# Optimization experiments

Measured on AMD Instinct MI355X. Metric: run time of the kernel, lower is better.

Reference implementation:

```python
import jax, jax.numpy as jnp
import numpy as np

K = 512
HIDDEN = 256


def setup_inputs() -> dict:
    key = jax.random.key(0)
    k1, k2 = jax.random.split(key)
    z = jax.random.normal(k1, (8, 8192, HIDDEN), dtype=jnp.float32)
    # codebook init: uniform(-1/k, 1/k) as in the torch module
    codebook = jax.random.uniform(k2, (K, HIDDEN), dtype=jnp.float32,
                                  minval=-1.0 / K, maxval=1.0 / K)
    return {"z": z, "codebook": codebook}


def reference(z, codebook):
    # squared L2 distance to every code, expanded form to avoid the
    # [N, k, hidden] intermediate: ||z||^2 - 2 z.c + ||c||^2
    z2 = jnp.sum(z * z, axis=-1, keepdims=True)            # [B, T, 1]
    c2 = jnp.sum(codebook * codebook, axis=-1)             # [k]
    cross = jnp.einsum('bth,kh->btk', z, codebook)         # [B, T, k]
    distances = z2 - 2.0 * cross + c2                      # [B, T, k]
    ind = jnp.argmin(distances, axis=-1)                   # [B, T] int
    z_q = codebook[ind]                                    # [B, T, hidden]

    vq_loss = jnp.mean((z_q - jax.lax.stop_gradient(z)) ** 2)
    commitment_loss = jnp.mean((z - jax.lax.stop_gradient(z_q)) ** 2)
    z_q_st = z + jax.lax.stop_gradient(z_q - z)
    return (z_q_st, ind, vq_loss + commitment_loss)
```

## Files before the change

### kernel.cpp

```cpp
#include <hip/hip_runtime.h>

#define M_TOKENS 65536
#define HID      256
#define KCODES   512

#define IND_OFF  (M_TOKENS * HID)
#define LOSS_OFF (IND_OFF + M_TOKENS)

#define TAU      1.5e-4f

#define WS_C2_OFF        16
#define WS_BHI_OFF       4096
#define WS_BLO_OFF       (4096 + 262144)
#define WS_LIST_OFF_FAST (4096 + 524288)
#define WS_LIST_OFF_SLOW 4096
#define WS_MIN_FAST      (WS_LIST_OFF_FAST + 8192 * 4)

typedef __attribute__((ext_vector_type(8))) short  short8;
typedef __attribute__((ext_vector_type(4))) float  f32x4;

__device__ inline unsigned short f2bf(float f) {
    unsigned u = __float_as_uint(f);
    u += 0x7FFF + ((u >> 16) & 1);
    return (unsigned short)(u >> 16);
}
__device__ inline float bf2f(unsigned short h) {
    return __uint_as_float(((unsigned)h) << 16);
}

__global__ __launch_bounds__(256) void vq_prep(
    const float* __restrict__ cb,
    unsigned short* __restrict__ Bhi, unsigned short* __restrict__ Blo,
    float* __restrict__ c2, double* __restrict__ acc, int* __restrict__ cnt) {
    int b = blockIdx.x;
    if (b < 64) {
        int g = b * 256 + threadIdx.x;
        int frag = g >> 6, lane = g & 63;
        int nb = frag >> 3, kb = frag & 7;
        int code = nb * 16 + (lane & 15);
        int kk = kb * 32 + (lane >> 4) * 8;
        const float4* s4 = reinterpret_cast<const float4*>(cb + code * HID + kk);
        float4 v0 = s4[0], v1 = s4[1];
        float f[8] = {v0.x, v0.y, v0.z, v0.w, v1.x, v1.y, v1.z, v1.w};
        short8 vh, vl;
        #pragma unroll
        for (int j = 0; j < 8; ++j) {
            unsigned short h = f2bf(f[j]);
            vh[j] = (short)h;
            vl[j] = (short)f2bf(f[j] - bf2f(h));
        }
        *reinterpret_cast<short8*>(Bhi + (size_t)g * 8) = vh;
        *reinterpret_cast<short8*>(Blo + (size_t)g * 8) = vl;
    } else {
        if (b == 64 && threadIdx.x == 0) { *acc = 0.0; *cnt = 0; }
        int k = (b - 64) * 256 + threadIdx.x;
        const float* row = cb + k * HID;
        double s = 0.0;
        for (int i = 0; i < HID; ++i) {
            double v = (double)row[i];
            s = fma(v, v, s);
        }
        c2[k] = (float)s;
    }
}

__global__ __launch_bounds__(256, 2) void vq_main_mfma(
    const float* __restrict__ z, const float* __restrict__ cb,
    const float* __restrict__ c2g,
    const unsigned short* __restrict__ Bhi,
    const unsigned short* __restrict__ Blo,
    float* __restrict__ out, double* __restrict__ loss_acc,
    int* __restrict__ cnt, int* __restrict__ list, int cap) {

    __shared__ short8 ldsB[2][32][64];
    __shared__ float  lds_c2[KCODES];

    const int tid  = threadIdx.x;
    const int wid  = tid >> 6;
    const int lane = tid & 63;
    const int q    = lane >> 4;
    const int tokW = blockIdx.x * 128 + wid * 32;

    const float4* z4  = reinterpret_cast<const float4*>(z);
    const float4* cb4 = reinterpret_cast<const float4*>(cb);

    lds_c2[tid]       = c2g[tid];
    lds_c2[tid + 256] = c2g[tid + 256];

#define STAGE(kv, bufv) do {                                                   \
        _Pragma("unroll")                                                      \
        for (int j = 0; j < 8; ++j) {                                          \
            int s_  = (wid << 3) | j;                                          \
            int g_  = s_ >> 4;                                                 \
            int t_  = s_ & 15;                                                 \
            int kb_ = t_ & 7;                                                  \
            const unsigned short* src_ =                                       \
                ((t_ < 8) ? Bhi : Blo) +                                       \
                (((size_t)((2 * (kv) + g_) * 8 + kb_) * 64 + lane) << 3);      \
            __builtin_amdgcn_global_load_lds(                                  \
                (const __attribute__((address_space(1))) void*)src_,           \
                (__attribute__((address_space(3))) void*)&ldsB[bufv][s_][0],   \
                16, 0, 0);                                                     \
        }                                                                      \
    } while (0)

    STAGE(0, 0);

    short8 ah[2][8], al[2][8];
    float sq[2];
    #pragma unroll
    for (int mf = 0; mf < 2; ++mf) {
        int token = tokW + mf * 16 + (lane & 15);
        const float4* zr = z4 + (size_t)token * 64 + q * 2;
        float s = 0.f;
        #pragma unroll
        for (int kb = 0; kb < 8; ++kb) {
            float4 v0 = zr[kb * 8];
            float4 v1 = zr[kb * 8 + 1];
            float f[8] = {v0.x, v0.y, v0.z, v0.w, v1.x, v1.y, v1.z, v1.w};
            short8 vh, vl;
            #pragma unroll
            for (int j = 0; j < 8; ++j) {
                unsigned short h = f2bf(f[j]);
                vh[j] = (short)h;
                vl[j] = (short)f2bf(f[j] - bf2f(h));
                s = fmaf(f[j], f[j], s);
            }
            ah[mf][kb] = vh;
            al[mf][kb] = vl;
        }
        s += __shfl_xor(s, 16, 64);
        s += __shfl_xor(s, 32, 64);
        sq[mf] = s;
    }

    float b1[2][4], b2[2][4];
    int   i1[2][4];
    #pragma unroll
    for (int mf = 0; mf < 2; ++mf)
        #pragma unroll
        for (int r = 0; r < 4; ++r) { b1[mf][r] = 3.4e38f; b2[mf][r] = 3.4e38f; i1[mf][r] = 0; }

    #pragma unroll 2
    for (int k = 0; k < 16; ++k) {
        int buf = k & 1;
        __syncthreads();
        if (k < 15) STAGE(k + 1, buf ^ 1);

        #pragma unroll
        for (int g = 0; g < 2; ++g) {
            f32x4 a0 = {0.f, 0.f, 0.f, 0.f};
            f32x4 a1 = {0.f, 0.f, 0.f, 0.f};
            __builtin_amdgcn_s_setprio(1);
            #pragma unroll
            for (int kb = 0; kb < 8; ++kb) {
                short8 vbh = ldsB[buf][g * 16 + kb][lane];
                short8 vbl = ldsB[buf][g * 16 + 8 + kb][lane];
                a0 = __builtin_amdgcn_mfma_f32_16x16x32_bf16(ah[0][kb], vbh, a0, 0, 0, 0);
                a1 = __builtin_amdgcn_mfma_f32_16x16x32_bf16(ah[1][kb], vbh, a1, 0, 0, 0);
                a0 = __builtin_amdgcn_mfma_f32_16x16x32_bf16(al[0][kb], vbh, a0, 0, 0, 0);
                a1 = __builtin_amdgcn_mfma_f32_16x16x32_bf16(al[1][kb], vbh, a1, 0, 0, 0);
                a0 = __builtin_amdgcn_mfma_f32_16x16x32_bf16(ah[0][kb], vbl, a0, 0, 0, 0);
                a1 = __builtin_amdgcn_mfma_f32_16x16x32_bf16(ah[1][kb], vbl, a1, 0, 0, 0);
            }
            __builtin_amdgcn_s_setprio(0);
            int code = (2 * k + g) * 16 + (lane & 15);
            float c2v = lds_c2[code];
            #pragma unroll
            for (int r = 0; r < 4; ++r) {
                float s0 = fmaf(-2.f, a0[r], c2v);
                if (s0 < b1[0][r]) { b2[0][r] = b1[0][r]; b1[0][r] = s0; i1[0][r] = code; }
                else if (s0 < b2[0][r]) b2[0][r] = s0;
                float s1 = fmaf(-2.f, a1[r], c2v);
                if (s1 < b1[1][r]) { b2[1][r] = b1[1][r]; b1[1][r] = s1; i1[1][r] = code; }
                else if (s1 < b2[1][r]) b2[1][r] = s1;
            }
        }
    }
#undef STAGE

    #pragma unroll
    for (int st = 1; st <= 8; st <<= 1) {
        #pragma unroll
        for (int mf = 0; mf < 2; ++mf)
            #pragma unroll
            for (int r = 0; r < 4; ++r) {
                float ob1 = __shfl_xor(b1[mf][r], st, 64);
                int   oi1 = __shfl_xor(i1[mf][r], st, 64);
                float ob2 = __shfl_xor(b2[mf][r], st, 64);
                if (ob1 < b1[mf][r] || (ob1 == b1[mf][r] && oi1 < i1[mf][r])) {
                    b2[mf][r] = fminf(b1[mf][r], ob2);
                    b1[mf][r] = ob1;
                    i1[mf][r] = oi1;
                } else {
                    b2[mf][r] = fminf(b2[mf][r], ob1);
                }
            }
    }

    if ((lane & 15) == 0) {
        #pragma unroll
        for (int mf = 0; mf < 2; ++mf) {
            float4 iv;
            #pragma unroll
            for (int r = 0; r < 4; ++r) {
                ((float*)&iv)[r] = (float)i1[mf][r];
                if (b2[mf][r] - b1[mf][r] <= TAU) {
                    int pos = atomicAdd(cnt, 1);
                    if (pos < cap) list[pos] = tokW + mf * 16 + q * 4 + r;
                }
            }
            *reinterpret_cast<float4*>(out + IND_OFF + tokW + mf * 16 + q * 4) = iv;
        }
    }

    double lsum = 0.0;
    #pragma unroll
    for (int mf = 0; mf < 2; ++mf)
        #pragma unroll
        for (int r = 0; r < 4; ++r) {
            float z2r = __shfl(sq[mf], (lane & 48) | (q * 4 + r), 64);
            if ((lane & 15) == 0) lsum += (double)z2r + (double)b1[mf][r];
        }
    lsum += __shfl_xor(lsum, 16, 64);
    lsum += __shfl_xor(lsum, 32, 64);
    if (lane == 0) atomicAdd(loss_acc, lsum);

    float4* out4 = reinterpret_cast<float4*>(out);
    #pragma unroll
    for (int tt = 0; tt < 32; ++tt) {
        int code = __shfl(i1[tt >> 4][tt & 3], ((tt >> 2) & 3) * 16, 64);
        float4 cv = cb4[(size_t)code * 64 + lane];
        out4[(size_t)(tokW + tt) * 64 + lane] = cv;
    }
}

#define BM   128
#define NC   128
#define KS   32
#define PAD  33

__global__ void vq_init(const float* __restrict__ cb, float* __restrict__ c2,
                        double* __restrict__ acc, int* __restrict__ cnt) {
    int k = threadIdx.x;
    if (k == 0) { *acc = 0.0; *cnt = 0; }
    const float* row = cb + k * HID;
    double s = 0.0;
    for (int i = 0; i < HID; ++i) {
        double v = (double)row[i];
        s = fma(v, v, s);
    }
    c2[k] = (float)s;
}

__global__ __launch_bounds__(256, 2) void vq_main_f32(
    const float* __restrict__ z, const float* __restrict__ cb,
    const float* __restrict__ c2g, float* __restrict__ out,
    double* __restrict__ loss_acc, int* __restrict__ cnt,
    int* __restrict__ list, int cap) {

    __shared__ float smem[(BM + NC) * PAD];
    float* zs = smem;
    float* cs = smem + BM * PAD;

    const int tid = threadIdx.x;
    const int tx = tid & 15;
    const int ty = tid >> 4;
    const int tokBase = blockIdx.x * BM;

    const float4* z4g  = reinterpret_cast<const float4*>(z);
    const float4* cb4g = reinterpret_cast<const float4*>(cb);

    float bs[8], bs2[8];
    int   bi[8];
    #pragma unroll
    for (int m = 0; m < 8; ++m) { bs[m] = 3.4e38f; bs2[m] = 3.4e38f; bi[m] = 0; }

    for (int chunk = 0; chunk < KCODES / NC; ++chunk) {
        float acc[8][8];
        #pragma unroll
        for (int m = 0; m < 8; ++m)
            #pragma unroll
            for (int n = 0; n < 8; ++n) acc[m][n] = 0.f;

        for (int ks = 0; ks < HID / KS; ++ks) {
            __syncthreads();
            #pragma unroll
            for (int i = 0; i < 4; ++i) {
                int f   = tid + i * 256;
                int row = f >> 3;
                int k4  = f & 7;
                float4 zv = z4g[(tokBase + row) * (HID / 4) + ks * (KS / 4) + k4];
                int b = row * PAD + k4 * 4;
                zs[b + 0] = zv.x; zs[b + 1] = zv.y; zs[b + 2] = zv.z; zs[b + 3] = zv.w;
                float4 cv = cb4g[(chunk * NC + row) * (HID / 4) + ks * (KS / 4) + k4];
                cs[b + 0] = cv.x; cs[b + 1] = cv.y; cs[b + 2] = cv.z; cs[b + 3] = cv.w;
            }
            __syncthreads();

            #pragma unroll 2
            for (int k = 0; k < KS; ++k) {
                float zf[8], cf[8];
                #pragma unroll
                for (int m = 0; m < 8; ++m) zf[m] = zs[(ty * 8 + m) * PAD + k];
                #pragma unroll
                for (int n = 0; n < 8; ++n) cf[n] = cs[(tx * 8 + n) * PAD + k];
                #pragma unroll
                for (int m = 0; m < 8; ++m)
                    #pragma unroll
                    for (int n = 0; n < 8; ++n)
                        acc[m][n] = fmaf(zf[m], cf[n], acc[m][n]);
            }
        }

        #pragma unroll
        for (int n = 0; n < 8; ++n) {
            int code = chunk * NC + tx * 8 + n;
            float c2v = c2g[code];
            #pragma unroll
            for (int m = 0; m < 8; ++m) {
                float s = fmaf(-2.f, acc[m][n], c2v);
                if (s < bs[m]) { bs2[m] = bs[m]; bs[m] = s; bi[m] = code; }
                else if (s < bs2[m]) bs2[m] = s;
            }
        }
    }

    __syncthreads();
    float* rs   = smem;
    int*   ri   = reinterpret_cast<int*>(smem + BM * 16);
    float* rs2  = smem + BM * 32;
    int*   inds = reinterpret_cast<int*>(smem + BM * 48);
    float* wred = smem + BM * 48 + BM;

    #pragma unroll
    for (int m = 0; m < 8; ++m) {
        int tok = ty * 8 + m;
        rs [tok * 16 + tx] = bs[m];
        ri [tok * 16 + tx] = bi[m];
        rs2[tok * 16 + tx] = bs2[m];
    }
    __syncthreads();

    if (tid < BM) {
        float B1 = rs[tid * 16];
        int   I1 = ri[tid * 16];
        float B2 = rs2[tid * 16];
        for (int j = 1; j < 16; ++j) {
            float b1v = rs [tid * 16 + j];
            int   i1v = ri [tid * 16 + j];
            float b2v = rs2[tid * 16 + j];
            if (b1v < B1 || (b1v == B1 && i1v < I1)) {
                B2 = fminf(B1, b2v); B1 = b1v; I1 = i1v;
            } else {
                B2 = fminf(B2, b1v);
            }
        }
        inds[tid] = I1;
        out[IND_OFF + tokBase + tid] = (float)I1;
        if (B2 - B1 <= TAU) {
            int pos = atomicAdd(cnt, 1);
            if (pos < cap) list[pos] = tokBase + tid;
        }
    }
    __syncthreads();

    float loc = 0.f;
    float4* out4 = reinterpret_cast<float4*>(out);
    for (int it = 0; it < (BM * HID / 4) / 256; ++it) {
        int e4  = it * 256 + tid;
        int tok = e4 >> 6;
        int h4  = e4 & 63;
        int code = inds[tok];
        float4 cv = cb4g[code * 64 + h4];
        float4 zv = z4g[(tokBase + tok) * 64 + h4];
        out4[(tokBase + tok) * 64 + h4] = cv;
        float dx = cv.x - zv.x, dy = cv.y - zv.y;
        float dz = cv.z - zv.z, dw = cv.w - zv.w;
        loc = fmaf(dx, dx, loc);
        loc = fmaf(dy, dy, loc);
        loc = fmaf(dz, dz, loc);
        loc = fmaf(dw, dw, loc);
    }
    #pragma unroll
    for (int off = 32; off > 0; off >>= 1) loc += __shfl_xor(loc, off, 64);
    int wave = tid >> 6;
    if ((tid & 63) == 0) wred[wave] = loc;
    __syncthreads();
    if (tid == 0) {
        double t = (double)wred[0] + (double)wred[1] +
                   (double)wred[2] + (double)wred[3];
        atomicAdd(loss_acc, t);
    }
}

__global__ __launch_bounds__(256) void vq_refine(
    const float* __restrict__ z, const float* __restrict__ cb,
    const float* __restrict__ c2g, const double* __restrict__ loss_acc,
    const int* __restrict__ cnt, const int* __restrict__ list,
    float* __restrict__ out, int cap) {

    if (blockIdx.x == 0 && threadIdx.x == 0)
        out[LOSS_OFF] = (float)(2.0 * (*loss_acc) / (double)(M_TOKENS * HID));

    __shared__ float  zrow[HID];
    __shared__ double red_d[256];
    __shared__ int    red_i[256];

    const int tid = threadIdx.x;
    int n = *cnt; if (n > cap) n = cap;

    for (int idx = blockIdx.x; idx < n; idx += gridDim.x) {
        int t = list[idx];
        float zi = z[t * HID + tid];
        zrow[tid] = zi;
        red_d[tid] = (double)zi * (double)zi;
        __syncthreads();
        for (int s = 128; s > 0; s >>= 1) {
            if (tid < s) red_d[tid] += red_d[tid + s];
            __syncthreads();
        }
        float z2f = (float)red_d[0];
        __syncthreads();

        const float4* zr4 = reinterpret_cast<const float4*>(zrow);
        const float4* c0  = reinterpret_cast<const float4*>(cb + tid * HID);
        const float4* c1  = reinterpret_cast<const float4*>(cb + (tid + 256) * HID);
        double p00 = 0, p01 = 0, p02 = 0, p03 = 0;
        double p10 = 0, p11 = 0, p12 = 0, p13 = 0;
        #pragma unroll 4
        for (int i = 0; i < HID / 4; ++i) {
            float4 zv = zr4[i];
            float4 a = c0[i];
            float4 b = c1[i];
            p00 = fma((double)zv.x, (double)a.x, p00);
            p01 = fma((double)zv.y, (double)a.y, p01);
            p02 = fma((double)zv.z, (double)a.z, p02);
            p03 = fma((double)zv.w, (double)a.w, p03);
            p10 = fma((double)zv.x, (double)b.x, p10);
            p11 = fma((double)zv.y, (double)b.y, p11);
            p12 = fma((double)zv.z, (double)b.z, p12);
            p13 = fma((double)zv.w, (double)b.w, p13);
        }
        double bestD = 1e300; int bestK = 1 << 30;
        #pragma unroll
        for (int c = 0; c < 2; ++c) {
            int k = tid + c * 256;
            double accd = (c == 0) ? ((p00 + p01) + (p02 + p03))
                                   : ((p10 + p11) + (p12 + p13));
            float cross32 = (float)accd;
            float u = 2.0f * cross32;
            float tq = (float)((double)z2f - (double)u);
            double v = (double)tq + (double)c2g[k];
            float D = (float)v;
            double Dd = (double)D;
            if (Dd < bestD || (Dd == bestD && k < bestK)) { bestD = Dd; bestK = k; }
        }
        red_d[tid] = bestD; red_i[tid] = bestK;
        __syncthreads();
        for (int s = 128; s > 0; s >>= 1) {
            if (tid < s) {
                double d2 = red_d[tid + s]; int i2 = red_i[tid + s];
                if (d2 < red_d[tid] || (d2 == red_d[tid] && i2 < red_i[tid])) {
                    red_d[tid] = d2; red_i[tid] = i2;
                }
            }
            __syncthreads();
        }
        int best = red_i[0];
        if (tid == 0) out[IND_OFF + t] = (float)best;
        out[t * HID + tid] = cb[best * HID + tid];
        __syncthreads();
    }
}

extern "C" void kernel_launch(void* const* d_in, const int* in_sizes, int n_in,
                              void* d_out, int out_size, void* d_ws, size_t ws_size,
                              hipStream_t stream) {
    const float* z  = (const float*)d_in[0];
    const float* cb = (const float*)d_in[1];
    float* out = (float*)d_out;
    double* acc = (double*)d_ws;
    int*  cnt = (int*)((char*)d_ws + 8);
    float* c2 = (float*)((char*)d_ws + WS_C2_OFF);

    if (ws_size >= WS_MIN_FAST) {
        unsigned short* Bhi = (unsigned short*)((char*)d_ws + WS_BHI_OFF);
        unsigned short* Blo = (unsigned short*)((char*)d_ws + WS_BLO_OFF);
        int* list = (int*)((char*)d_ws + WS_LIST_OFF_FAST);
        int cap = 8192;
        vq_prep<<<66, 256, 0, stream>>>(cb, Bhi, Blo, c2, acc, cnt);
        vq_main_mfma<<<M_TOKENS / 128, 256, 0, stream>>>(
            z, cb, c2, Bhi, Blo, out, acc, cnt, list, cap);
        vq_refine<<<256, 256, 0, stream>>>(z, cb, c2, acc, cnt, list, out, cap);
    } else {
        int* list = (int*)((char*)d_ws + WS_LIST_OFF_SLOW);
        int cap = 0;
        if (ws_size > WS_LIST_OFF_SLOW + 16) {
            size_t avail = (ws_size - WS_LIST_OFF_SLOW) / 4;
            cap = (avail > 8192) ? 8192 : (int)avail;
        }
        vq_init<<<1, 512, 0, stream>>>(cb, c2, acc, cnt);
        vq_main_f32<<<M_TOKENS / BM, 256, 0, stream>>>(
            z, cb, c2, out, acc, cnt, list, cap);
        vq_refine<<<256, 256, 0, stream>>>(z, cb, c2, acc, cnt, list, out, cap);
    }
}
```

Baseline: 176.4 us.

## Batch eight tokens per block in refine kernel to reuse codebook loads

The refine kernel now processes eight ambiguous tokens per block iteration. Each codebook row is loaded once and applied to all eight tokens held in shared memory, instead of being reloaded for every token. The per-token reductions are batched so one set of barriers serves all eight, and the grid is halved to 128 blocks. This amortises codebook traffic and synchronisation, but it raises register and shared-memory use, which may lower occupancy, and it lowers parallelism when the list of tokens is short.

Result: no change. 177.7 us (+0.7%).

```diff
diff --git a/kernel.cpp b/kernel.cpp
--- a/kernel.cpp
+++ b/kernel.cpp
@@ -394,6 +394,7 @@
     }
 }
 
+#define RT 8
 __global__ __launch_bounds__(256) void vq_refine(
     const float* __restrict__ z, const float* __restrict__ cb,
     const float* __restrict__ c2g, const double* __restrict__ loss_acc,
@@ -403,73 +404,95 @@
     if (blockIdx.x == 0 && threadIdx.x == 0)
         out[LOSS_OFF] = (float)(2.0 * (*loss_acc) / (double)(M_TOKENS * HID));
 
-    __shared__ float  zrow[HID];
-    __shared__ double red_d[256];
-    __shared__ int    red_i[256];
+    __shared__ float  zrow[RT][HID];
+    __shared__ double redd[RT][256];
+    __shared__ int    redi[RT][256];
 
     const int tid = threadIdx.x;
     int n = *cnt; if (n > cap) n = cap;
 
-    for (int idx = blockIdx.x; idx < n; idx += gridDim.x) {
-        int t = list[idx];
-        float zi = z[t * HID + tid];
-        zrow[tid] = zi;
-        red_d[tid] = (double)zi * (double)zi;
-        __syncthreads();
-        for (int s = 128; s > 0; s >>= 1) {
-            if (tid < s) red_d[tid] += red_d[tid + s];
-            __syncthreads();
-        }
-        float z2f = (float)red_d[0];
-        __syncthreads();
-
-        const float4* zr4 = reinterpret_cast<const float4*>(zrow);
-        const float4* c0  = reinterpret_cast<const float4*>(cb + tid * HID);
-        const float4* c1  = reinterpret_cast<const float4*>(cb + (tid + 256) * HID);
-        double p00 = 0, p01 = 0, p02 = 0, p03 = 0;
-        double p10 = 0, p11 = 0, p12 = 0, p13 = 0;
-        #pragma unroll 4
-        for (int i = 0; i < HID / 4; ++i) {
-            float4 zv = zr4[i];
-            float4 a = c0[i];
-            float4 b = c1[i];
-            p00 = fma((double)zv.x, (double)a.x, p00);
-            p01 = fma((double)zv.y, (double)a.y, p01);
-            p02 = fma((double)zv.z, (double)a.z, p02);
-            p03 = fma((double)zv.w, (double)a.w, p03);
-            p10 = fma((double)zv.x, (double)b.x, p10);
-            p11 = fma((double)zv.y, (double)b.y, p11);
-            p12 = fma((double)zv.z, (double)b.z, p12);
-            p13 = fma((double)zv.w, (double)b.w, p13);
-        }
-        double bestD = 1e300; int bestK = 1 << 30;
-        #pragma unroll
-        for (int c = 0; c < 2; ++c) {
-            int k = tid + c * 256;
-            double accd = (c == 0) ? ((p00 + p01) + (p02 + p03))
-                                   : ((p10 + p11) + (p12 + p13));
-            float cross32 = (float)accd;
-            float u = 2.0f * cross32;
-            float tq = (float)((double)z2f - (double)u);
-            double v = (double)tq + (double)c2g[k];
-            float D = (float)v;
-            double Dd = (double)D;
-            if (Dd < bestD || (Dd == bestD && k < bestK)) { bestD = Dd; bestK = k; }
-        }
-        red_d[tid] = bestD; red_i[tid] = bestK;
+    for (int base = blockIdx.x * RT; base < n; base += gridDim.x * RT) {
+        int toks[RT];
+        #pragma unroll
+        for (int t = 0; t < RT; ++t) {
+            int ii = base + t;
+            if (ii > n - 1) ii = n - 1;
+            toks[t] = list[ii];
+        }
+        #pragma unroll
+        for (int t = 0; t < RT; ++t) {
+            float v = z[(size_t)toks[t] * HID + tid];
+            zrow[t][tid] = v;
+            redd[t][tid] = (double)v * (double)v;
+        }
         __syncthreads();
         for (int s = 128; s > 0; s >>= 1) {
             if (tid < s) {
-                double d2 = red_d[tid + s]; int i2 = red_i[tid + s];
-                if (d2 < red_d[tid] || (d2 == red_d[tid] && i2 < red_i[tid])) {
-                    red_d[tid] = d2; red_i[tid] = i2;
+                #pragma unroll
+                for (int t = 0; t < RT; ++t) redd[t][tid] += redd[t][tid + s];
+            }
+            __syncthreads();
+        }
+        float z2f[RT];
+        #pragma unroll
+        for (int t = 0; t < RT; ++t) z2f[t] = (float)redd[t][0];
+        __syncthreads();
+
+        double bd[RT];
+        int    bk[RT];
+        #pragma unroll
+        for (int t = 0; t < RT; ++t) { bd[t] = 1e300; bk[t] = 1 << 30; }
+
+        for (int c = 0; c < 2; ++c) {
+            int k = tid + c * 256;
+            const float4* cr = reinterpret_cast<const float4*>(cb + (size_t)k * HID);
+            double acc[RT];
+            #pragma unroll
+            for (int t = 0; t < RT; ++t) acc[t] = 0.0;
+            for (int i = 0; i < HID / 4; ++i) {
+                float4 cv = cr[i];
+                #pragma unroll
+                for (int t = 0; t < RT; ++t) {
+                    float4 zv = *reinterpret_cast<const float4*>(&zrow[t][i * 4]);
+                    acc[t] = fma((double)zv.x, (double)cv.x, acc[t]);
+                    acc[t] = fma((double)zv.y, (double)cv.y, acc[t]);
+                    acc[t] = fma((double)zv.z, (double)cv.z, acc[t]);
+                    acc[t] = fma((double)zv.w, (double)cv.w, acc[t]);
                 }
             }
+            float c2v = c2g[k];
+            #pragma unroll
+            for (int t = 0; t < RT; ++t) {
+                float cross32 = (float)acc[t];
+                float u = 2.0f * cross32;
+                float tq = (float)((double)z2f[t] - (double)u);
+                float D = (float)((double)tq + (double)c2v);
+                double Dd = (double)D;
+                if (Dd < bd[t] || (Dd == bd[t] && k < bk[t])) { bd[t] = Dd; bk[t] = k; }
+            }
+        }
+        #pragma unroll
+        for (int t = 0; t < RT; ++t) { redd[t][tid] = bd[t]; redi[t][tid] = bk[t]; }
+        __syncthreads();
+        for (int s = 128; s > 0; s >>= 1) {
+            if (tid < s) {
+                #pragma unroll
+                for (int t = 0; t < RT; ++t) {
+                    double d2 = redd[t][tid + s]; int i2v = redi[t][tid + s];
+                    if (d2 < redd[t][tid] ||
+                        (d2 == redd[t][tid] && i2v < redi[t][tid])) {
+                        redd[t][tid] = d2; redi[t][tid] = i2v;
+                    }
+                }
+            }
             __syncthreads();
         }
-        int best = red_i[0];
-        if (tid == 0) out[IND_OFF + t] = (float)best;
-        out[t * HID + tid] = cb[best * HID + tid];
+        if (tid < RT) out[IND_OFF + toks[tid]] = (float)redi[tid][0];
+        #pragma unroll
+        for (int t = 0; t < RT; ++t) {
+            int best = redi[t][0];
+            out[(size_t)toks[t] * HID + tid] = cb[(size_t)best * HID + tid];
+        }
         __syncthreads();
     }
 }
@@ -492,7 +515,7 @@
         vq_prep<<<66, 256, 0, stream>>>(cb, Bhi, Blo, c2, acc, cnt);
         vq_main_mfma<<<M_TOKENS / 128, 256, 0, stream>>>(
             z, cb, c2, Bhi, Blo, out, acc, cnt, list, cap);
-        vq_refine<<<256, 256, 0, stream>>>(z, cb, c2, acc, cnt, list, out, cap);
+        vq_refine<<<128, 256, 0, stream>>>(z, cb, c2, acc, cnt, list, out, cap);
     } else {
         int* list = (int*)((char*)d_ws + WS_LIST_OFF_SLOW);
         int cap = 0;
@@ -503,6 +526,6 @@
         vq_init<<<1, 512, 0, stream>>>(cb, c2, acc, cnt);
         vq_main_f32<<<M_TOKENS / BM, 256, 0, stream>>>(
             z, cb, c2, out, acc, cnt, list, cap);
-        vq_refine<<<256, 256, 0, stream>>>(z, cb, c2, acc, cnt, list, out, cap);
-    }
-}
+        vq_refine<<<128, 256, 0, stream>>>(z, cb, c2, acc, cnt, list, out, cap);
+    }
+}
```
